# Kernel optimization log

Measured on AMD Instinct MI355X. Metric: run time of the kernel, lower is better.

## Reference

```python
import jax, jax.numpy as jnp
import numpy as np

N_GENES = 8192      # input genes
WM = 4              # width_multiplier: hidden nodes per gene
HID = N_GENES * WM  # 32768 hidden units
N_TF = 1024         # embedding dim (TF activities)
GPT = 64            # target genes per TF in the prior network
BATCH = 256
EPS = 1e-5          # BatchNorm1d eps


def _connectivity():
    # layer1: hidden node h belongs to gene h // WM (fan_in = 1)
    rows1 = np.arange(HID, dtype=np.int32)
    cols1 = (rows1 // WM).astype(np.int32)
    # layer2: fully connected within each gene group (WM x WM blocks)
    rows2 = np.repeat(np.arange(HID, dtype=np.int32), WM)
    cols2 = (((np.arange(HID)[:, None] // WM) * WM) + np.arange(WM)).astype(np.int32).ravel()
    # layer3: each TF connects to all WM nodes of GPT randomly chosen genes
    rng = np.random.default_rng(0)
    genes = rng.integers(0, N_GENES, size=(N_TF, GPT))
    cols3 = (genes[:, :, None] * WM + np.arange(WM)).astype(np.int32).reshape(-1)
    rows3 = np.repeat(np.arange(N_TF, dtype=np.int32), GPT * WM)
    return rows1, cols1, rows2, cols2, rows3, cols3


def _sparse_linear(x, w, b, rows, cols, out_dim):
    # y[b, o] = sum_{e: rows[e]==o} w[e] * x[b, cols[e]] + b[o]
    xe = x[:, cols] * w  # [B, E]
    y = jnp.zeros((x.shape[0], out_dim), x.dtype).at[:, rows].add(xe)
    return y + b


def _batchnorm(x):
    # BatchNorm1d(affine=False), training mode: biased batch var
    m = jnp.mean(x, axis=0)
    v = jnp.var(x, axis=0)
    return (x - m) / jnp.sqrt(v + EPS)


def setup_inputs() -> dict:
    key = jax.random.key(0)
    k = jax.random.split(key, 7)
    rows1, cols1, rows2, cols2, rows3, cols3 = _connectivity()
    inp = {
        "features": jax.random.normal(k[0], (BATCH, N_GENES), jnp.float32),
        "w1": jax.random.normal(k[1], (HID,), jnp.float32),                 # fan_in 1
        "b1": jax.random.normal(k[2], (HID,), jnp.float32) * 0.01,
        "w2": jax.random.normal(k[3], (HID * WM,), jnp.float32) / np.sqrt(WM),
        "b2": jax.random.normal(k[4], (HID,), jnp.float32) * 0.01,
        "w3": jax.random.normal(k[5], (N_TF * GPT * WM,), jnp.float32) / np.sqrt(GPT * WM),
        "b3": jax.random.normal(k[6], (N_TF,), jnp.float32) * 0.01,
        "rows1": jnp.asarray(rows1), "cols1": jnp.asarray(cols1),
        "rows2": jnp.asarray(rows2), "cols2": jnp.asarray(cols2),
        "rows3": jnp.asarray(rows3), "cols3": jnp.asarray(cols3),
    }
    return inp


def reference(features, w1, b1, w2, b2, w3, b3,
              rows1, cols1, rows2, cols2, rows3, cols3):
    h = _sparse_linear(features, w1, b1, rows1, cols1, HID)
    h = _batchnorm(jax.nn.relu(h))
    h = _sparse_linear(h, w2, b2, rows2, cols2, HID)
    h = _batchnorm(jax.nn.relu(h))
    z = _sparse_linear(h, w3, b3, rows3, cols3, N_TF)
    return _batchnorm(z)
```

## Files before the change

kernel.cpp:

```cpp
#include <hip/hip_runtime.h>
#include <cstddef>

#define EPS 1e-5f

constexpr int NG  = 8192;
constexpr int HID = 32768;
constexpr int NTF = 1024;
constexpr int B   = 256;

static __device__ __forceinline__ unsigned short f2bf(float v) {
    union { float f; unsigned u; } a; a.f = v;
    unsigned r = a.u + 0x7fffu + ((a.u >> 16) & 1u);
    return (unsigned short)(r >> 16);
}

__global__ __launch_bounds__(256) void fused12(
    const float* __restrict__ x,
    const float* __restrict__ w1,
    const float* __restrict__ b1,
    const float* __restrict__ w2,
    const float* __restrict__ b2,
    unsigned short* __restrict__ h2b,
    float* __restrict__ m2g,
    float* __restrict__ inv2g)
{
    const int lane  = threadIdx.x & 63;
    const int slice = threadIdx.x >> 6;
    const int c     = (blockIdx.x << 6) + lane;
    const int g     = c >> 2;
    const int b0    = slice << 6;

    __shared__ float redA[4][64], redB[4][64];
    __shared__ float m1s[64], inv1s[64];

    const float w1c = w1[c], b1c = b1[c];
    const float* xp = x + (size_t)b0 * NG + g;

    float s = 0.f, s2 = 0.f;
    #pragma unroll 8
    for (int i = 0; i < 64; ++i) {
        float h = fmaxf(fmaf(w1c, xp[(size_t)i * NG], b1c), 0.f);
        s += h;
        s2 = fmaf(h, h, s2);
    }
    redA[slice][lane] = s;
    redB[slice][lane] = s2;
    __syncthreads();
    if (slice == 0) {
        float S  = redA[0][lane] + redA[1][lane] + redA[2][lane] + redA[3][lane];
        float S2 = redB[0][lane] + redB[1][lane] + redB[2][lane] + redB[3][lane];
        float m  = S * (1.f / 256.f);
        float v  = fmaf(-m, m, S2 * (1.f / 256.f));
        m1s[lane]   = m;
        inv1s[lane] = rsqrtf(v + EPS);
    }
    __syncthreads();

    const int lbase = lane & ~3;
    const int gbase = g << 2;
    float w1j[4], b1j[4], w2s[4];
    float bconst = b2[c];
    #pragma unroll
    for (int j = 0; j < 4; ++j) {
        w1j[j] = w1[gbase + j];
        b1j[j] = b1[gbase + j];
        float wv = w2[(c << 2) + j] * inv1s[lbase + j];
        w2s[j] = wv;
        bconst = fmaf(-wv, m1s[lbase + j], bconst);
    }

    float t2s = 0.f, t2s2 = 0.f;
    unsigned short* op = h2b + ((size_t)slice * HID + c) * 64;
    for (int i0 = 0; i0 < 64; i0 += 4) {
        ushort4 pk;
        unsigned short* pp = (unsigned short*)&pk;
        #pragma unroll
        for (int u = 0; u < 4; ++u) {
            float v = xp[(size_t)(i0 + u) * NG];
            float acc = bconst;
            #pragma unroll
            for (int j = 0; j < 4; ++j) {
                float r = fmaxf(fmaf(w1j[j], v, b1j[j]), 0.f);
                acc = fmaf(w2s[j], r, acc);
            }
            float r2 = fmaxf(acc, 0.f);
            t2s += r2;
            t2s2 = fmaf(r2, r2, t2s2);
            pp[u] = f2bf(r2);
        }
        *(ushort4*)(op + i0) = pk;
    }

    __syncthreads();
    redA[slice][lane] = t2s;
    redB[slice][lane] = t2s2;
    __syncthreads();
    if (slice == 0) {
        float S  = redA[0][lane] + redA[1][lane] + redA[2][lane] + redA[3][lane];
        float S2 = redB[0][lane] + redB[1][lane] + redB[2][lane] + redB[3][lane];
        float m  = S * (1.f / 256.f);
        float v  = fmaf(-m, m, S2 * (1.f / 256.f));
        m2g[c]   = m;
        inv2g[c] = rsqrtf(v + EPS);
    }
}

__global__ __launch_bounds__(256) void fused3(
    const unsigned short* __restrict__ h2,
    const float* __restrict__ m2g,
    const float* __restrict__ inv2g,
    const float* __restrict__ w3,
    const float* __restrict__ b3,
    const int*   __restrict__ cols3,
    float* __restrict__ out)
{
    const int t   = blockIdx.x;
    const int tid = threadIdx.x;

    __shared__ float wls[256];
    __shared__ int   als[64];
    __shared__ float wred[4], rs[4], rs2[4];
    __shared__ float accq[32][64];
    __shared__ float red2[4][64];
    __shared__ float zs[256];

    int   col = cols3[(t << 8) + tid];
    float wv  = w3[(t << 8) + tid] * inv2g[col];
    wls[tid]  = wv;
    if (tid < 64) als[tid] = cols3[(t << 8) + (tid << 2)] << 7;
    float bp  = wv * m2g[col];
    #pragma unroll
    for (int o = 32; o > 0; o >>= 1) bp += __shfl_xor(bp, o);
    if ((tid & 63) == 0) wred[tid >> 6] = bp;
    __syncthreads();

    const char* h2c  = (const char*)h2;
    const int   lrow = (tid & 7) << 3;

    for (int bt = 0; bt < 4; ++bt) {
        float a0=0.f,a1=0.f,a2=0.f,a3=0.f,a4=0.f,a5=0.f,a6=0.f,a7=0.f;
        const char* bpt = h2c + (size_t)bt * ((size_t)HID * 128) + ((tid & 31) << 4);
        #pragma unroll
        for (int jb = 0; jb < 8; ++jb) {
            const int   j = (jb << 3) + (tid >> 5);
            const float w = wls[(jb << 5) + (tid >> 3)];
            const uint4 u = *(const uint4*)(bpt + als[j]);
            union { unsigned v; float f; } p0,p1,p2,p3,p4,p5,p6,p7;
            p0.v = u.x << 16; p1.v = u.x & 0xffff0000u;
            p2.v = u.y << 16; p3.v = u.y & 0xffff0000u;
            p4.v = u.z << 16; p5.v = u.z & 0xffff0000u;
            p6.v = u.w << 16; p7.v = u.w & 0xffff0000u;
            a0 = fmaf(w, p0.f, a0); a1 = fmaf(w, p1.f, a1);
            a2 = fmaf(w, p2.f, a2); a3 = fmaf(w, p3.f, a3);
            a4 = fmaf(w, p4.f, a4); a5 = fmaf(w, p5.f, a5);
            a6 = fmaf(w, p6.f, a6); a7 = fmaf(w, p7.f, a7);
        }
        __syncthreads();
        *(float4*)&accq[tid >> 3][lrow]     = make_float4(a0, a1, a2, a3);
        *(float4*)&accq[tid >> 3][lrow + 4] = make_float4(a4, a5, a6, a7);
        __syncthreads();
        {
            const int r = tid & 63, gq = tid >> 6;
            float p = 0.f;
            #pragma unroll
            for (int i = 0; i < 8; ++i) p += accq[(gq << 3) + i][r];
            red2[gq][r] = p;
        }
        __syncthreads();
        if (tid < 64)
            zs[(bt << 6) + tid] = red2[0][tid] + red2[1][tid]
                                + red2[2][tid] + red2[3][tid];
    }
    __syncthreads();

    const float zbias = b3[t] - (wred[0] + wred[1] + wred[2] + wred[3]);
    float z = zs[tid] + zbias;

    float s = z, s2 = z * z;
    #pragma unroll
    for (int o = 32; o > 0; o >>= 1) {
        s  += __shfl_xor(s, o);
        s2 += __shfl_xor(s2, o);
    }
    if ((tid & 63) == 0) { rs[tid >> 6] = s; rs2[tid >> 6] = s2; }
    __syncthreads();
    float S  = rs[0] + rs[1] + rs[2] + rs[3];
    float S2 = rs2[0] + rs2[1] + rs2[2] + rs2[3];
    float m  = S * (1.f / 256.f);
    float v  = fmaf(-m, m, S2 * (1.f / 256.f));
    float invs = rsqrtf(v + EPS);
    out[(size_t)tid * NTF + t] = (z - m) * invs;
}

extern "C" void kernel_launch(void* const* d_in, const int* in_sizes, int n_in,
                              void* d_out, int out_size, void* d_ws, size_t ws_size,
                              hipStream_t stream) {
    const float* x   = (const float*)d_in[0];
    const float* w1  = (const float*)d_in[1];
    const float* b1  = (const float*)d_in[2];
    const float* w2  = (const float*)d_in[3];
    const float* b2  = (const float*)d_in[4];
    const float* w3  = (const float*)d_in[5];
    const float* b3  = (const float*)d_in[6];
    const int* cols3 = (const int*)d_in[12];
    float* out = (float*)d_out;

    unsigned short* h2b = (unsigned short*)d_ws;
    float* m2g   = (float*)(h2b + (size_t)HID * B);
    float* inv2g = m2g + HID;

    fused12<<<HID / 64, 256, 0, stream>>>(x, w1, b1, w2, b2, h2b, m2g, inv2g);
    fused3<<<NTF, 256, 0, stream>>>(h2b, m2g, inv2g, w3, b3, cols3, out);
}
```

Baseline: 117.4 us.

## Halve fused12 block width and cache feature loads in registers

Each fused12 block now covers 32 hidden columns with 8 row slices of 32 batch rows instead of 64 columns with 4 slices, which doubles the grid size. Each thread keeps its 32 input values in a register array, so the second pass reads registers instead of reloading x from global memory. The aim is to drop the repeated global reads and add more blocks for parallelism. The costs are higher register pressure and half-wavefront lane mappings (32-lane groups on 64-wide wavefronts), which may hurt coalescing and give narrower stores.

```diff
diff --git a/kernel.cpp b/kernel.cpp
--- a/kernel.cpp
+++ b/kernel.cpp
@@ -24,35 +24,39 @@
     float* __restrict__ m2g,
     float* __restrict__ inv2g)
 {
-    const int lane  = threadIdx.x & 63;
-    const int slice = threadIdx.x >> 6;
-    const int c     = (blockIdx.x << 6) + lane;
+    const int lane  = threadIdx.x & 31;
+    const int slice = threadIdx.x >> 5;
+    const int c     = (blockIdx.x << 5) + lane;
     const int g     = c >> 2;
-    const int b0    = slice << 6;
-
-    __shared__ float redA[4][64], redB[4][64];
-    __shared__ float m1s[64], inv1s[64];
+    const int r0    = slice << 5;
+
+    __shared__ float redA[8][32], redB[8][32];
+    __shared__ float m1s[32], inv1s[32];
 
     const float w1c = w1[c], b1c = b1[c];
-    const float* xp = x + (size_t)b0 * NG + g;
-
+    const float* xp = x + (size_t)r0 * NG + g;
+
+    float xv[32];
     float s = 0.f, s2 = 0.f;
-    #pragma unroll 8
-    for (int i = 0; i < 64; ++i) {
-        float h = fmaxf(fmaf(w1c, xp[(size_t)i * NG], b1c), 0.f);
+    #pragma unroll
+    for (int i = 0; i < 32; ++i) {
+        float v = xp[(size_t)i * NG];
+        xv[i] = v;
+        float h = fmaxf(fmaf(w1c, v, b1c), 0.f);
         s += h;
         s2 = fmaf(h, h, s2);
     }
     redA[slice][lane] = s;
     redB[slice][lane] = s2;
     __syncthreads();
-    if (slice == 0) {
-        float S  = redA[0][lane] + redA[1][lane] + redA[2][lane] + redA[3][lane];
-        float S2 = redB[0][lane] + redB[1][lane] + redB[2][lane] + redB[3][lane];
-        float m  = S * (1.f / 256.f);
-        float v  = fmaf(-m, m, S2 * (1.f / 256.f));
-        m1s[lane]   = m;
-        inv1s[lane] = rsqrtf(v + EPS);
+    if (threadIdx.x < 32) {
+        float S = 0.f, S2 = 0.f;
+        #pragma unroll
+        for (int k = 0; k < 8; ++k) { S += redA[k][threadIdx.x]; S2 += redB[k][threadIdx.x]; }
+        float m = S * (1.f / 256.f);
+        float v = fmaf(-m, m, S2 * (1.f / 256.f));
+        m1s[threadIdx.x]   = m;
+        inv1s[threadIdx.x] = rsqrtf(v + EPS);
     }
     __syncthreads();
 
@@ -70,13 +74,15 @@
     }
 
     float t2s = 0.f, t2s2 = 0.f;
-    unsigned short* op = h2b + ((size_t)slice * HID + c) * 64;
-    for (int i0 = 0; i0 < 64; i0 += 4) {
+    const int bt = slice >> 1;
+    const int rr = (slice & 1) << 5;
+    unsigned short* op = h2b + ((size_t)bt * HID + c) * 64 + rr;
+    for (int i0 = 0; i0 < 32; i0 += 4) {
         ushort4 pk;
         unsigned short* pp = (unsigned short*)&pk;
         #pragma unroll
         for (int u = 0; u < 4; ++u) {
-            float v = xp[(size_t)(i0 + u) * NG];
+            float v = xv[i0 + u];
             float acc = bconst;
             #pragma unroll
             for (int j = 0; j < 4; ++j) {
@@ -95,13 +101,15 @@
     redA[slice][lane] = t2s;
     redB[slice][lane] = t2s2;
     __syncthreads();
-    if (slice == 0) {
-        float S  = redA[0][lane] + redA[1][lane] + redA[2][lane] + redA[3][lane];
-        float S2 = redB[0][lane] + redB[1][lane] + redB[2][lane] + redB[3][lane];
-        float m  = S * (1.f / 256.f);
-        float v  = fmaf(-m, m, S2 * (1.f / 256.f));
-        m2g[c]   = m;
-        inv2g[c] = rsqrtf(v + EPS);
+    if (threadIdx.x < 32) {
+        float S = 0.f, S2 = 0.f;
+        #pragma unroll
+        for (int k = 0; k < 8; ++k) { S += redA[k][threadIdx.x]; S2 += redB[k][threadIdx.x]; }
+        float m = S * (1.f / 256.f);
+        float v = fmaf(-m, m, S2 * (1.f / 256.f));
+        const int cw = (blockIdx.x << 5) + threadIdx.x;
+        m2g[cw]   = m;
+        inv2g[cw] = rsqrtf(v + EPS);
     }
 }
 
@@ -209,6 +217,6 @@
     float* m2g   = (float*)(h2b + (size_t)HID * B);
     float* inv2g = m2g + HID;
 
-    fused12<<<HID / 64, 256, 0, stream>>>(x, w1, b1, w2, b2, h2b, m2g, inv2g);
+    fused12<<<HID / 32, 256, 0, stream>>>(x, w1, b1, w2, b2, h2b, m2g, inv2g);
     fused3<<<NTF, 256, 0, stream>>>(h2b, m2g, inv2g, w3, b3, cols3, out);
 }
```

Measured after the change: 114.8 us. -2.2%, faster.
